# Performance work log

Measured on AMD Instinct MI355X. Metric: run time of the kernel, lower is better.

## Reference

```python
import jax, jax.numpy as jnp
import numpy as np
import math

DIM = 768
HEADS = 8
DIM_HEAD = 64
INNER = HEADS * DIM_HEAD  # 512
B, L = 2, 4096
LN_EPS = 1e-5


def setup_inputs() -> dict:
    key = jax.random.key(0)
    ks = jax.random.split(key, 6)
    std = 0.02
    return {
        "x": jax.random.normal(ks[0], (B, L, DIM), dtype=jnp.float32),
        "ln_gamma": jnp.ones((DIM,), dtype=jnp.float32),
        "ln_beta": jnp.zeros((DIM,), dtype=jnp.float32),
        "Wq": jax.random.normal(ks[1], (DIM, INNER), dtype=jnp.float32) * std,
        "Wkv": jax.random.normal(ks[2], (DIM, 2 * INNER), dtype=jnp.float32) * std,
        "Wo": jax.random.normal(ks[3], (INNER, DIM), dtype=jnp.float32) * std,
    }


def reference(x, ln_gamma, ln_beta, Wq, Wkv, Wo):
    b, l, _ = x.shape
    # LayerNorm (eps=1e-5, affine)
    mu = jnp.mean(x, axis=-1, keepdims=True)
    var = jnp.mean(jnp.square(x - mu), axis=-1, keepdims=True)
    xn = (x - mu) * jax.lax.rsqrt(var + LN_EPS) * ln_gamma + ln_beta

    q = xn @ Wq                      # (b, l, inner)
    kv = xn @ Wkv                    # (b, l, 2*inner)
    k, v = jnp.split(kv, 2, axis=-1)

    def to_heads(t):
        return t.reshape(b, l, HEADS, DIM_HEAD).transpose(0, 2, 1, 3)  # (b,h,l,d)

    q, k, v = to_heads(q), to_heads(k), to_heads(v)

    scale = 1.0 / math.sqrt(math.sqrt(DIM_HEAD))
    # explicit quadratic scores, softmax in float32 as in original
    weight = jnp.einsum("bhid,bhjd->bhij", q * scale, k * scale)
    weight = jax.nn.softmax(weight.astype(jnp.float32), axis=-1).astype(q.dtype)
    out = jnp.einsum("bhij,bhjd->bhid", weight, v)       # (b,h,l,d)
    out = out.transpose(0, 2, 1, 3).reshape(b, l, INNER)  # merge heads
    return out @ Wo
```

## Files before the change

kernel.cpp:

```cpp
#include <hip/hip_runtime.h>
#include <hip/hip_bf16.h>


typedef __bf16 bf16_t;
typedef __bf16 bf16x4 __attribute__((ext_vector_type(4)));
typedef __bf16 bf16x8 __attribute__((ext_vector_type(8)));
typedef float f32x4 __attribute__((ext_vector_type(4)));
typedef unsigned int u32x2 __attribute__((ext_vector_type(2)));

#define MFMA16(a, b, c) __builtin_amdgcn_mfma_f32_16x16x32_bf16((a), (b), (c), 0, 0, 0)

#define QSCALE 0.18033688011112042f

#define GLDS(gp, lp)                                                          \
    __builtin_amdgcn_global_load_lds(                                         \
        (const __attribute__((address_space(1))) void*)(gp),                  \
        (__attribute__((address_space(3))) void*)(lp), 16, 0, 0)

__device__ __forceinline__ int detect_f32(const unsigned int* __restrict__ xw) {
    const int l = threadIdx.x & 63;
    int cnt = 0;
#pragma unroll
    for (int j = 0; j < 2; ++j) {
        const unsigned int e = (xw[l * 2 + j] >> 7) & 0xFF;
        cnt += (e >= 100 && e <= 140) ? 1 : 0;
    }
#pragma unroll
    for (int off = 1; off < 64; off <<= 1) cnt += __shfl_xor(cnt, off, 64);
    return cnt < 64;
}

__global__ __launch_bounds__(256) void prep_kernel(
    const void* __restrict__ xv, const void* __restrict__ gv,
    const void* __restrict__ bv, const void* __restrict__ wq,
    const void* __restrict__ wkv, const void* __restrict__ wo,
    bf16_t* __restrict__ xn, bf16_t* __restrict__ WqkvT, bf16_t* __restrict__ WoT,
    int* __restrict__ flag) {
    const int f32 = detect_f32((const unsigned int*)xv);
    const int bid = blockIdx.x;
    const int t = threadIdx.x;
    if (bid == 0 && t == 0) *flag = f32;

    __shared__ bf16_t Ts[64 * 68];

    if (bid < 2048) {
        const int lane = t & 63;
        const int row = bid * 4 + (t >> 6);
        const int c0 = lane * 12;
        float v[12];
        if (f32) {
            const float* xr = (const float*)xv + (size_t)row * 768 + c0;
#pragma unroll
            for (int i = 0; i < 3; ++i) {
                const float4 q = *(const float4*)(xr + i * 4);
                v[i * 4] = q.x; v[i * 4 + 1] = q.y;
                v[i * 4 + 2] = q.z; v[i * 4 + 3] = q.w;
            }
        } else {
            const bf16_t* xr = (const bf16_t*)xv + (size_t)row * 768 + c0;
#pragma unroll
            for (int i = 0; i < 3; ++i) {
                const bf16x4 q = *(const bf16x4*)(xr + i * 4);
#pragma unroll
                for (int j = 0; j < 4; ++j) v[i * 4 + j] = (float)q[j];
            }
        }
        float s = 0.f, sq = 0.f;
#pragma unroll
        for (int j = 0; j < 12; ++j) { s += v[j]; sq += v[j] * v[j]; }
#pragma unroll
        for (int off = 1; off < 64; off <<= 1) {
            s += __shfl_xor(s, off, 64);
            sq += __shfl_xor(sq, off, 64);
        }
        const float mu = s * (1.0f / 768.0f);
        const float var = sq * (1.0f / 768.0f) - mu * mu;
        const float rstd = rsqrtf(var + 1e-5f);

        bf16_t* xo = xn + (size_t)row * 768 + c0;
#pragma unroll
        for (int i = 0; i < 3; ++i) {
            bf16x4 o;
#pragma unroll
            for (int j = 0; j < 4; ++j) {
                const int c = c0 + i * 4 + j;
                const float gc = f32 ? ((const float*)gv)[c] : (float)((const bf16_t*)gv)[c];
                const float bc = f32 ? ((const float*)bv)[c] : (float)((const bf16_t*)bv)[c];
                o[j] = (bf16_t)((v[i * 4 + j] - mu) * rstd * gc + bc);
            }
            *(bf16x4*)(xo + i * 4) = o;
        }
        return;
    }

    int idx = bid - 2048;
    const void* in;
    bf16_t* out;
    int R, C, cx, ry;
    if (idx < 96) {
        in = wq; out = WqkvT; R = 768; C = 512;
        cx = idx & 7; ry = idx >> 3;
    } else if (idx < 288) {
        idx -= 96;
        in = wkv; out = WqkvT + (size_t)512 * 768; R = 768; C = 1024;
        cx = idx & 15; ry = idx >> 4;
    } else {
        idx -= 288;
        in = wo; out = WoT; R = 512; C = 768;
        cx = idx % 12; ry = idx / 12;
    }
    const int r0 = ry * 64, c0 = cx * 64;
    {
        const int r = t >> 2, c = (t & 3) * 16;
        if (f32) {
            const float* src = (const float*)in + (size_t)(r0 + r) * C + c0 + c;
#pragma unroll
            for (int i = 0; i < 16; i += 4) {
                const float4 q = *(const float4*)(src + i);
                Ts[r * 68 + c + i] = (bf16_t)q.x;
                Ts[r * 68 + c + i + 1] = (bf16_t)q.y;
                Ts[r * 68 + c + i + 2] = (bf16_t)q.z;
                Ts[r * 68 + c + i + 3] = (bf16_t)q.w;
            }
        } else {
            const bf16_t* src = (const bf16_t*)in + (size_t)(r0 + r) * C + c0 + c;
            *(bf16x8*)&Ts[r * 68 + c] = *(const bf16x8*)src;
            *(bf16x8*)&Ts[r * 68 + c + 8] = *(const bf16x8*)(src + 8);
        }
    }
    __syncthreads();
    {
        const int oc = t >> 2, seg = (t & 3) * 16;
        bf16x8 v0, v1;
#pragma unroll
        for (int j = 0; j < 8; ++j) v0[j] = Ts[(seg + j) * 68 + oc];
#pragma unroll
        for (int j = 0; j < 8; ++j) v1[j] = Ts[(seg + 8 + j) * 68 + oc];
        bf16_t* dst = out + (size_t)(c0 + oc) * R + r0 + seg;
        *(bf16x8*)dst = v0;
        *(bf16x8*)(dst + 8) = v1;
    }
}

__global__ __launch_bounds__(256) void qkv_gemm(const bf16_t* __restrict__ A,
                                                const bf16_t* __restrict__ BT,
                                                bf16_t* __restrict__ qkv,
                                                bf16_t* __restrict__ vtg,
                                                int M, int N, int K) {
    const int m0 = blockIdx.y * 128;
    const int n0 = blockIdx.x * 128;
    __shared__ bf16_t As[128 * 32];
    __shared__ bf16_t Bs[128 * 32];

    const int t = threadIdx.x;
    const int lane = t & 63;
    const int w = t >> 6;
    const int wm = (w >> 1) * 64;
    const int wn = (w & 1) * 64;
    const int quad = lane >> 4;
    const int cl = lane & 15;

    f32x4 acc[4][4];
    const f32x4 z4 = {0.f, 0.f, 0.f, 0.f};
#pragma unroll
    for (int mi = 0; mi < 4; ++mi)
#pragma unroll
        for (int ni = 0; ni < 4; ++ni) acc[mi][ni] = z4;

    const int r0 = lane >> 2;
    const int c0 = (lane & 3) * 8;
    const bf16_t* AgL = A + (size_t)(m0 + w * 32 + r0) * K + c0;
    const bf16_t* AgH = A + (size_t)(m0 + w * 32 + 16 + r0) * K + c0;
    const bf16_t* BgL = BT + (size_t)(n0 + w * 32 + r0) * K + c0;
    const bf16_t* BgH = BT + (size_t)(n0 + w * 32 + 16 + r0) * K + c0;
    bf16_t* AdL = &As[(w * 32) * 32];
    bf16_t* AdH = &As[(w * 32 + 16) * 32];
    bf16_t* BdL = &Bs[(w * 32) * 32];
    bf16_t* BdH = &Bs[(w * 32 + 16) * 32];

    for (int kt = 0; kt < K; kt += 32) {
        __syncthreads();
        GLDS(AgL + kt, AdL);
        GLDS(AgH + kt, AdH);
        GLDS(BgL + kt, BdL);
        GLDS(BgH + kt, BdH);
        __syncthreads();

        const int ko = quad * 8;
        bf16x8 af[4], bfr[4];
#pragma unroll
        for (int mi = 0; mi < 4; ++mi)
            af[mi] = *(const bf16x8*)&As[(wm + mi * 16 + cl) * 32 + ko];
#pragma unroll
        for (int ni = 0; ni < 4; ++ni)
            bfr[ni] = *(const bf16x8*)&Bs[(wn + ni * 16 + cl) * 32 + ko];
#pragma unroll
        for (int mi = 0; mi < 4; ++mi)
#pragma unroll
            for (int ni = 0; ni < 4; ++ni)
                acc[mi][ni] = MFMA16(af[mi], bfr[ni], acc[mi][ni]);
    }

    if (n0 >= 1024) {
        const int b = m0 >> 12;
#pragma unroll
        for (int mi = 0; mi < 4; ++mi) {
#pragma unroll
            for (int ni = 0; ni < 4; ++ni) {
                const int tok = (m0 & 4095) + wm + mi * 16 + quad * 4;
                const int dl = n0 + wn + ni * 16 + cl - 1024;
                bf16x4 pk;
#pragma unroll
                for (int r4 = 0; r4 < 4; ++r4) pk[r4] = (bf16_t)acc[mi][ni][r4];
                *(bf16x4*)(vtg + ((size_t)(b * 8 + (dl >> 6)) * 64 + (dl & 63)) * 4096 +
                           tok) = pk;
            }
        }
    } else {
        const float sc = (n0 < 512) ? QSCALE : 1.0f;
#pragma unroll
        for (int mi = 0; mi < 4; ++mi) {
#pragma unroll
            for (int ni = 0; ni < 4; ++ni) {
#pragma unroll
                for (int r4 = 0; r4 < 4; ++r4) {
                    const int row = m0 + wm + mi * 16 + quad * 4 + r4;
                    const int col = n0 + wn + ni * 16 + cl;
                    qkv[(size_t)row * N + col] = (bf16_t)(acc[mi][ni][r4] * sc);
                }
            }
        }
    }
}

__global__ __launch_bounds__(128) void gemm_bt64(const bf16_t* __restrict__ A,
                                                 const bf16_t* __restrict__ BT,
                                                 void* __restrict__ C,
                                                 int M, int N, int K,
                                                 const int* __restrict__ out_flag) {
    const int m0 = blockIdx.y * 128;
    const int n0 = blockIdx.x * 64;
    __shared__ bf16_t As[128 * 32];
    __shared__ bf16_t Bs[64 * 32];

    const int t = threadIdx.x;
    const int lane = t & 63;
    const int w = t >> 6;
    const int quad = lane >> 4;
    const int cl = lane & 15;

    f32x4 acc[4][4];
    const f32x4 z4 = {0.f, 0.f, 0.f, 0.f};
#pragma unroll
    for (int mi = 0; mi < 4; ++mi)
#pragma unroll
        for (int ni = 0; ni < 4; ++ni) acc[mi][ni] = z4;

    const int r0 = lane >> 2;
    const int c0 = (lane & 3) * 8;
    const bf16_t* Ag = A + (size_t)(m0 + w * 64 + r0) * K + c0;
    const bf16_t* Bg = BT + (size_t)(n0 + w * 32 + r0) * K + c0;
    bf16_t* Ad = &As[(w * 64) * 32];
    bf16_t* Bd = &Bs[(w * 32) * 32];

    for (int kt = 0; kt < K; kt += 32) {
        __syncthreads();
#pragma unroll
        for (int i = 0; i < 4; ++i) GLDS(Ag + kt + (size_t)i * 16 * K, Ad + i * 512);
#pragma unroll
        for (int i = 0; i < 2; ++i) GLDS(Bg + kt + (size_t)i * 16 * K, Bd + i * 512);
        __syncthreads();

        const int ko = quad * 8;
        bf16x8 af[4], bfr[4];
#pragma unroll
        for (int mi = 0; mi < 4; ++mi)
            af[mi] = *(const bf16x8*)&As[(w * 64 + mi * 16 + cl) * 32 + ko];
#pragma unroll
        for (int ni = 0; ni < 4; ++ni)
            bfr[ni] = *(const bf16x8*)&Bs[(ni * 16 + cl) * 32 + ko];
#pragma unroll
        for (int mi = 0; mi < 4; ++mi)
#pragma unroll
            for (int ni = 0; ni < 4; ++ni)
                acc[mi][ni] = MFMA16(af[mi], bfr[ni], acc[mi][ni]);
    }

    const int f32out = *out_flag;
#pragma unroll
    for (int mi = 0; mi < 4; ++mi) {
#pragma unroll
        for (int ni = 0; ni < 4; ++ni) {
#pragma unroll
            for (int r4 = 0; r4 < 4; ++r4) {
                const int row = m0 + w * 64 + mi * 16 + quad * 4 + r4;
                const int col = n0 + ni * 16 + cl;
                if (f32out)
                    ((float*)C)[(size_t)row * N + col] = acc[mi][ni][r4];
                else
                    ((bf16_t*)C)[(size_t)row * N + col] = (bf16_t)acc[mi][ni][r4];
            }
        }
    }
}

__global__ __launch_bounds__(256, 2) void attn_kernel(const bf16_t* __restrict__ qkv,
                                                      const bf16_t* __restrict__ vtg,
                                                      bf16_t* __restrict__ ao) {
    const int qt = blockIdx.x;
    const int bh = blockIdx.y;
    const int b = bh >> 3, h = bh & 7;
    const int q0 = qt * 128;

    __shared__ bf16_t Ps[4][64 * 68];
    __shared__ bf16_t Ks[2][64 * 68];
    __shared__ bf16_t Vs[2][64 * 68];

    const int t = threadIdx.x;
    const int lane = t & 63;
    const int w = t >> 6;
    const int qsub = w & 1;
    const int kh = w >> 1;
    const int quad = lane >> 4;
    const int cl = lane & 15;

    const size_t rowbase = (size_t)b * 4096;
    const int qcol = h * 64;
    const int kcol = 512 + h * 64;

    bf16_t* Qtr = &Ps[0][0];
    {
        const bf16_t* qsrc = qkv + (rowbase + q0 + w * 32) * 1536 + qcol;
#pragma unroll
        for (int i = 0; i < 4; ++i)
            GLDS(qsrc + (size_t)(i * 8 + (lane >> 3)) * 1536 + (lane & 7) * 8,
                 Qtr + (w * 32 + i * 8) * 64);
    }
    __syncthreads();

    bf16x8 aq[4][2];
#pragma unroll
    for (int rt = 0; rt < 4; ++rt)
#pragma unroll
        for (int hh = 0; hh < 2; ++hh)
            aq[rt][hh] =
                *(const bf16x8*)&Qtr[(qsub * 64 + rt * 16 + cl) * 64 + hh * 32 + quad * 8];

    bf16x8 ones;
#pragma unroll
    for (int e = 0; e < 8; ++e) ones[e] = (bf16_t)1.0f;

    const f32x4 z4 = {0.f, 0.f, 0.f, 0.f};
    f32x4 o[4][4];
    f32x4 l_acc[4];
#pragma unroll
    for (int rt = 0; rt < 4; ++rt) {
        l_acc[rt] = z4;
#pragma unroll
        for (int ni = 0; ni < 4; ++ni) o[rt][ni] = z4;
    }

    const int t2 = qsub * 64 + lane;
    const int sr = t2 >> 1;
    const int sh = (t2 & 1) * 32;

    bf16x8 kreg[4], vreg[4];
    {
        const int k0 = kh * 2048;
        const bf16_t* ks = qkv + (rowbase + k0 + sr) * 1536 + kcol + sh;
        const bf16_t* vs = vtg + ((size_t)bh * 64 + sr) * 4096 + k0 + sh;
#pragma unroll
        for (int o8 = 0; o8 < 4; ++o8) {
            kreg[o8] = *(const bf16x8*)(ks + o8 * 8);
            vreg[o8] = *(const bf16x8*)(vs + o8 * 8);
        }
    }

    for (int it = 0; it < 32; ++it) {
        __syncthreads();
#pragma unroll
        for (int o8 = 0; o8 < 4; ++o8) {
            *(bf16x8*)&Ks[kh][sr * 68 + sh + o8 * 8] = kreg[o8];
            *(bf16x8*)&Vs[kh][sr * 68 + sh + o8 * 8] = vreg[o8];
        }
        __syncthreads();

        if (it < 31) {
            const int k0n = kh * 2048 + (it + 1) * 64;
            const bf16_t* ks = qkv + (rowbase + k0n + sr) * 1536 + kcol + sh;
            const bf16_t* vs = vtg + ((size_t)bh * 64 + sr) * 4096 + k0n + sh;
#pragma unroll
            for (int o8 = 0; o8 < 4; ++o8) {
                kreg[o8] = *(const bf16x8*)(ks + o8 * 8);
                vreg[o8] = *(const bf16x8*)(vs + o8 * 8);
            }
        }

        const int ko = quad * 8;
        bf16x8 kb[4][2];
#pragma unroll
        for (int ni = 0; ni < 4; ++ni) {
            kb[ni][0] = *(const bf16x8*)&Ks[kh][(ni * 16 + cl) * 68 + ko];
            kb[ni][1] = *(const bf16x8*)&Ks[kh][(ni * 16 + cl) * 68 + 32 + ko];
        }
        __builtin_amdgcn_s_setprio(1);
#pragma unroll
        for (int rt = 0; rt < 4; ++rt) {
#pragma unroll
            for (int ni = 0; ni < 4; ++ni) {
                f32x4 s = z4;
                s = MFMA16(kb[ni][0], aq[rt][0], s);
                s = MFMA16(kb[ni][1], aq[rt][1], s);
                const float e0 = __builtin_amdgcn_exp2f(s[0]);
                const float e1 = __builtin_amdgcn_exp2f(s[1]);
                const float e2 = __builtin_amdgcn_exp2f(s[2]);
                const float e3 = __builtin_amdgcn_exp2f(s[3]);
                u32x2 pk;
                asm("v_cvt_pk_bf16_f32 %0, %1, %2" : "=v"(pk[0]) : "v"(e0), "v"(e1));
                asm("v_cvt_pk_bf16_f32 %0, %1, %2" : "=v"(pk[1]) : "v"(e2), "v"(e3));
                *(u32x2*)&Ps[w][(rt * 16 + cl) * 68 + ni * 16 + quad * 4] = pk;
            }
        }
        __builtin_amdgcn_s_setprio(0);

        bf16x8 vb[4][2];
#pragma unroll
        for (int ni = 0; ni < 4; ++ni) {
            vb[ni][0] = *(const bf16x8*)&Vs[kh][(ni * 16 + cl) * 68 + ko];
            vb[ni][1] = *(const bf16x8*)&Vs[kh][(ni * 16 + cl) * 68 + 32 + ko];
        }
        __builtin_amdgcn_s_setprio(1);
#pragma unroll
        for (int rt = 0; rt < 4; ++rt) {
            const bf16x8 p0 = *(const bf16x8*)&Ps[w][(rt * 16 + cl) * 68 + ko];
            const bf16x8 p1 = *(const bf16x8*)&Ps[w][(rt * 16 + cl) * 68 + 32 + ko];
#pragma unroll
            for (int ni = 0; ni < 4; ++ni) {
                o[rt][ni] = MFMA16(p0, vb[ni][0], o[rt][ni]);
                o[rt][ni] = MFMA16(p1, vb[ni][1], o[rt][ni]);
            }
            l_acc[rt] = MFMA16(p0, ones, l_acc[rt]);
            l_acc[rt] = MFMA16(p1, ones, l_acc[rt]);
        }
        __builtin_amdgcn_s_setprio(0);
    }

    float* cb = (float*)&Ps[0][0];
    __syncthreads();
    if (kh == 1) {
#pragma unroll
        for (int rt = 0; rt < 4; ++rt) {
#pragma unroll
            for (int r4 = 0; r4 < 4; ++r4) {
                const int row = rt * 16 + quad * 4 + r4;
                float* rp = cb + qsub * 4160 + row * 65;
#pragma unroll
                for (int ni = 0; ni < 4; ++ni) rp[ni * 16 + cl] = o[rt][ni][r4];
                if (cl == 0) rp[64] = l_acc[rt][r4];
            }
        }
    }
    __syncthreads();
    if (kh == 0) {
#pragma unroll
        for (int rt = 0; rt < 4; ++rt) {
#pragma unroll
            for (int r4 = 0; r4 < 4; ++r4) {
                const int row = rt * 16 + quad * 4 + r4;
                const float* rp = cb + qsub * 4160 + row * 65;
                const float inv = 1.0f / (l_acc[rt][r4] + rp[64]);
                const size_t orow = rowbase + q0 + qsub * 64 + row;
#pragma unroll
                for (int ni = 0; ni < 4; ++ni)
                    ao[orow * 512 + h * 64 + ni * 16 + cl] =
                        (bf16_t)((o[rt][ni][r4] + rp[ni * 16 + cl]) * inv);
            }
        }
    }
}

extern "C" void kernel_launch(void* const* d_in, const int* in_sizes, int n_in,
                              void* d_out, int out_size, void* d_ws, size_t ws_size,
                              hipStream_t stream) {
    const void* x = d_in[0];
    const void* gamma = d_in[1];
    const void* beta = d_in[2];
    const void* Wq = d_in[3];
    const void* Wkv = d_in[4];
    const void* Wo = d_in[5];

    char* wsb = (char*)d_ws;
    int* flag = (int*)wsb;
    bf16_t* xn = (bf16_t*)(wsb + 256);
    bf16_t* WqkvT = xn + (size_t)8192 * 768;
    bf16_t* WoT = WqkvT + (size_t)1536 * 768;
    bf16_t* qkv = WoT + (size_t)768 * 512;
    bf16_t* aob = xn;
    bf16_t* vtg = (bf16_t*)d_out;

    prep_kernel<<<2432, 256, 0, stream>>>(x, gamma, beta, Wq, Wkv, Wo, xn, WqkvT, WoT,
                                          flag);

    qkv_gemm<<<dim3(12, 64), 256, 0, stream>>>(xn, WqkvT, qkv, vtg, 8192, 1536, 768);

    attn_kernel<<<dim3(32, 16), 256, 0, stream>>>(qkv, vtg, aob);

    gemm_bt64<<<dim3(12, 64), 128, 0, stream>>>(aob, WoT, d_out, 8192, 768, 512, flag);
}
```

Before: 231.5 us.

## Shrink attention q-tile to 64 rows and drop split-K across warps

```diff
diff --git a/kernel.cpp b/kernel.cpp
--- a/kernel.cpp
+++ b/kernel.cpp
@@ -304,23 +304,21 @@
     }
 }
 
-__global__ __launch_bounds__(256, 2) void attn_kernel(const bf16_t* __restrict__ qkv,
+__global__ __launch_bounds__(256, 4) void attn_kernel(const bf16_t* __restrict__ qkv,
                                                       const bf16_t* __restrict__ vtg,
                                                       bf16_t* __restrict__ ao) {
     const int qt = blockIdx.x;
     const int bh = blockIdx.y;
     const int b = bh >> 3, h = bh & 7;
-    const int q0 = qt * 128;
-
-    __shared__ bf16_t Ps[4][64 * 68];
-    __shared__ bf16_t Ks[2][64 * 68];
-    __shared__ bf16_t Vs[2][64 * 68];
+    const int q0 = qt * 64;
+
+    __shared__ bf16_t Ps[4][16 * 68];
+    __shared__ bf16_t Ks[64 * 68];
+    __shared__ bf16_t Vs[64 * 68];
 
     const int t = threadIdx.x;
     const int lane = t & 63;
     const int w = t >> 6;
-    const int qsub = w & 1;
-    const int kh = w >> 1;
     const int quad = lane >> 4;
     const int cl = lane & 15;
 
@@ -328,154 +326,104 @@
     const int qcol = h * 64;
     const int kcol = 512 + h * 64;
 
-    bf16_t* Qtr = &Ps[0][0];
+    bf16_t* Qtr = &Ks[0];
     {
-        const bf16_t* qsrc = qkv + (rowbase + q0 + w * 32) * 1536 + qcol;
-#pragma unroll
-        for (int i = 0; i < 4; ++i)
+        const bf16_t* qsrc = qkv + (rowbase + q0 + w * 16) * 1536 + qcol;
+#pragma unroll
+        for (int i = 0; i < 2; ++i)
             GLDS(qsrc + (size_t)(i * 8 + (lane >> 3)) * 1536 + (lane & 7) * 8,
-                 Qtr + (w * 32 + i * 8) * 64);
-    }
+                 Qtr + (w * 16 + i * 8) * 64);
+    }
+
+    const int sr2 = t >> 3;
+    const int sh2 = (t & 7) * 8;
+    const bf16_t* kgp = qkv + (rowbase + sr2) * 1536 + kcol + sh2;
+    const bf16_t* vgp = vtg + ((size_t)bh * 64 + sr2) * 4096 + sh2;
+
+    bf16x8 kreg[2], vreg[2];
+    {
+        kreg[0] = *(const bf16x8*)(kgp);
+        kreg[1] = *(const bf16x8*)(kgp + (size_t)32 * 1536);
+        vreg[0] = *(const bf16x8*)(vgp);
+        vreg[1] = *(const bf16x8*)(vgp + (size_t)32 * 4096);
+    }
+
     __syncthreads();
 
-    bf16x8 aq[4][2];
-#pragma unroll
-    for (int rt = 0; rt < 4; ++rt)
-#pragma unroll
-        for (int hh = 0; hh < 2; ++hh)
-            aq[rt][hh] =
-                *(const bf16x8*)&Qtr[(qsub * 64 + rt * 16 + cl) * 64 + hh * 32 + quad * 8];
+    bf16x8 aq[2];
+#pragma unroll
+    for (int hh = 0; hh < 2; ++hh)
+        aq[hh] = *(const bf16x8*)&Qtr[(w * 16 + cl) * 64 + hh * 32 + quad * 8];
 
     bf16x8 ones;
 #pragma unroll
     for (int e = 0; e < 8; ++e) ones[e] = (bf16_t)1.0f;
 
     const f32x4 z4 = {0.f, 0.f, 0.f, 0.f};
-    f32x4 o[4][4];
-    f32x4 l_acc[4];
-#pragma unroll
-    for (int rt = 0; rt < 4; ++rt) {
-        l_acc[rt] = z4;
-#pragma unroll
-        for (int ni = 0; ni < 4; ++ni) o[rt][ni] = z4;
-    }
-
-    const int t2 = qsub * 64 + lane;
-    const int sr = t2 >> 1;
-    const int sh = (t2 & 1) * 32;
-
-    bf16x8 kreg[4], vreg[4];
-    {
-        const int k0 = kh * 2048;
-        const bf16_t* ks = qkv + (rowbase + k0 + sr) * 1536 + kcol + sh;
-        const bf16_t* vs = vtg + ((size_t)bh * 64 + sr) * 4096 + k0 + sh;
-#pragma unroll
-        for (int o8 = 0; o8 < 4; ++o8) {
-            kreg[o8] = *(const bf16x8*)(ks + o8 * 8);
-            vreg[o8] = *(const bf16x8*)(vs + o8 * 8);
-        }
-    }
-
-    for (int it = 0; it < 32; ++it) {
-        __syncthreads();
-#pragma unroll
-        for (int o8 = 0; o8 < 4; ++o8) {
-            *(bf16x8*)&Ks[kh][sr * 68 + sh + o8 * 8] = kreg[o8];
-            *(bf16x8*)&Vs[kh][sr * 68 + sh + o8 * 8] = vreg[o8];
-        }
-        __syncthreads();
-
-        if (it < 31) {
-            const int k0n = kh * 2048 + (it + 1) * 64;
-            const bf16_t* ks = qkv + (rowbase + k0n + sr) * 1536 + kcol + sh;
-            const bf16_t* vs = vtg + ((size_t)bh * 64 + sr) * 4096 + k0n + sh;
-#pragma unroll
-            for (int o8 = 0; o8 < 4; ++o8) {
-                kreg[o8] = *(const bf16x8*)(ks + o8 * 8);
-                vreg[o8] = *(const bf16x8*)(vs + o8 * 8);
-            }
-        }
-
-        const int ko = quad * 8;
-        bf16x8 kb[4][2];
+    f32x4 o[4];
+    f32x4 l_acc = z4;
+#pragma unroll
+    for (int ni = 0; ni < 4; ++ni) o[ni] = z4;
+
+    for (int it = 0; it < 64; ++it) {
+        __syncthreads();
+        *(bf16x8*)&Ks[sr2 * 68 + sh2] = kreg[0];
+        *(bf16x8*)&Ks[(sr2 + 32) * 68 + sh2] = kreg[1];
+        *(bf16x8*)&Vs[sr2 * 68 + sh2] = vreg[0];
+        *(bf16x8*)&Vs[(sr2 + 32) * 68 + sh2] = vreg[1];
+        __syncthreads();
+
+        if (it < 63) {
+            const size_t ko = (size_t)(it + 1) * 64;
+            kreg[0] = *(const bf16x8*)(kgp + ko * 1536);
+            kreg[1] = *(const bf16x8*)(kgp + (ko + 32) * 1536);
+            vreg[0] = *(const bf16x8*)(vgp + ko);
+            vreg[1] = *(const bf16x8*)(vgp + (size_t)32 * 4096 + ko);
+        }
+
+        const int ko2 = quad * 8;
+        __builtin_amdgcn_s_setprio(1);
 #pragma unroll
         for (int ni = 0; ni < 4; ++ni) {
-            kb[ni][0] = *(const bf16x8*)&Ks[kh][(ni * 16 + cl) * 68 + ko];
-            kb[ni][1] = *(const bf16x8*)&Ks[kh][(ni * 16 + cl) * 68 + 32 + ko];
-        }
+            const bf16x8 kb0 = *(const bf16x8*)&Ks[(ni * 16 + cl) * 68 + ko2];
+            const bf16x8 kb1 = *(const bf16x8*)&Ks[(ni * 16 + cl) * 68 + 32 + ko2];
+            f32x4 s = z4;
+            s = MFMA16(kb0, aq[0], s);
+            s = MFMA16(kb1, aq[1], s);
+            const float e0 = __builtin_amdgcn_exp2f(s[0]);
+            const float e1 = __builtin_amdgcn_exp2f(s[1]);
+            const float e2 = __builtin_amdgcn_exp2f(s[2]);
+            const float e3 = __builtin_amdgcn_exp2f(s[3]);
+            u32x2 pk;
+            asm("v_cvt_pk_bf16_f32 %0, %1, %2" : "=v"(pk[0]) : "v"(e0), "v"(e1));
+            asm("v_cvt_pk_bf16_f32 %0, %1, %2" : "=v"(pk[1]) : "v"(e2), "v"(e3));
+            *(u32x2*)&Ps[w][cl * 68 + ni * 16 + quad * 4] = pk;
+        }
+        __builtin_amdgcn_s_setprio(0);
+
+        const bf16x8 p0 = *(const bf16x8*)&Ps[w][cl * 68 + ko2];
+        const bf16x8 p1 = *(const bf16x8*)&Ps[w][cl * 68 + 32 + ko2];
         __builtin_amdgcn_s_setprio(1);
 #pragma unroll
-        for (int rt = 0; rt < 4; ++rt) {
-#pragma unroll
-            for (int ni = 0; ni < 4; ++ni) {
-                f32x4 s = z4;
-                s = MFMA16(kb[ni][0], aq[rt][0], s);
-                s = MFMA16(kb[ni][1], aq[rt][1], s);
-                const float e0 = __builtin_amdgcn_exp2f(s[0]);
-                const float e1 = __builtin_amdgcn_exp2f(s[1]);
-                const float e2 = __builtin_amdgcn_exp2f(s[2]);
-                const float e3 = __builtin_amdgcn_exp2f(s[3]);
-                u32x2 pk;
-                asm("v_cvt_pk_bf16_f32 %0, %1, %2" : "=v"(pk[0]) : "v"(e0), "v"(e1));
-                asm("v_cvt_pk_bf16_f32 %0, %1, %2" : "=v"(pk[1]) : "v"(e2), "v"(e3));
-                *(u32x2*)&Ps[w][(rt * 16 + cl) * 68 + ni * 16 + quad * 4] = pk;
-            }
-        }
+        for (int ni = 0; ni < 4; ++ni) {
+            const bf16x8 vb0 = *(const bf16x8*)&Vs[(ni * 16 + cl) * 68 + ko2];
+            const bf16x8 vb1 = *(const bf16x8*)&Vs[(ni * 16 + cl) * 68 + 32 + ko2];
+            o[ni] = MFMA16(p0, vb0, o[ni]);
+            o[ni] = MFMA16(p1, vb1, o[ni]);
+        }
+        l_acc = MFMA16(p0, ones, l_acc);
+        l_acc = MFMA16(p1, ones, l_acc);
         __builtin_amdgcn_s_setprio(0);
-
-        bf16x8 vb[4][2];
-#pragma unroll
-        for (int ni = 0; ni < 4; ++ni) {
-            vb[ni][0] = *(const bf16x8*)&Vs[kh][(ni * 16 + cl) * 68 + ko];
-            vb[ni][1] = *(const bf16x8*)&Vs[kh][(ni * 16 + cl) * 68 + 32 + ko];
-        }
-        __builtin_amdgcn_s_setprio(1);
-#pragma unroll
-        for (int rt = 0; rt < 4; ++rt) {
-            const bf16x8 p0 = *(const bf16x8*)&Ps[w][(rt * 16 + cl) * 68 + ko];
-            const bf16x8 p1 = *(const bf16x8*)&Ps[w][(rt * 16 + cl) * 68 + 32 + ko];
-#pragma unroll
-            for (int ni = 0; ni < 4; ++ni) {
-                o[rt][ni] = MFMA16(p0, vb[ni][0], o[rt][ni]);
-                o[rt][ni] = MFMA16(p1, vb[ni][1], o[rt][ni]);
-            }
-            l_acc[rt] = MFMA16(p0, ones, l_acc[rt]);
-            l_acc[rt] = MFMA16(p1, ones, l_acc[rt]);
-        }
-        __builtin_amdgcn_s_setprio(0);
-    }
-
-    float* cb = (float*)&Ps[0][0];
-    __syncthreads();
-    if (kh == 1) {
-#pragma unroll
-        for (int rt = 0; rt < 4; ++rt) {
-#pragma unroll
-            for (int r4 = 0; r4 < 4; ++r4) {
-                const int row = rt * 16 + quad * 4 + r4;
-                float* rp = cb + qsub * 4160 + row * 65;
-#pragma unroll
-                for (int ni = 0; ni < 4; ++ni) rp[ni * 16 + cl] = o[rt][ni][r4];
-                if (cl == 0) rp[64] = l_acc[rt][r4];
-            }
-        }
-    }
-    __syncthreads();
-    if (kh == 0) {
-#pragma unroll
-        for (int rt = 0; rt < 4; ++rt) {
-#pragma unroll
-            for (int r4 = 0; r4 < 4; ++r4) {
-                const int row = rt * 16 + quad * 4 + r4;
-                const float* rp = cb + qsub * 4160 + row * 65;
-                const float inv = 1.0f / (l_acc[rt][r4] + rp[64]);
-                const size_t orow = rowbase + q0 + qsub * 64 + row;
-#pragma unroll
-                for (int ni = 0; ni < 4; ++ni)
-                    ao[orow * 512 + h * 64 + ni * 16 + cl] =
-                        (bf16_t)((o[rt][ni][r4] + rp[ni * 16 + cl]) * inv);
-            }
-        }
+    }
+
+#pragma unroll
+    for (int r4 = 0; r4 < 4; ++r4) {
+        const int row = q0 + w * 16 + quad * 4 + r4;
+        const float inv = 1.0f / l_acc[r4];
+        bf16_t* op = ao + (rowbase + row) * 512 + qcol;
+#pragma unroll
+        for (int ni = 0; ni < 4; ++ni)
+            op[ni * 16 + cl] = (bf16_t)(o[ni][r4] * inv);
     }
 }
 
@@ -503,7 +451,7 @@
 
     qkv_gemm<<<dim3(12, 64), 256, 0, stream>>>(xn, WqkvT, qkv, vtg, 8192, 1536, 768);
 
-    attn_kernel<<<dim3(32, 16), 256, 0, stream>>>(qkv, vtg, aob);
+    attn_kernel<<<dim3(64, 16), 256, 0, stream>>>(qkv, vtg, aob);
 
     gemm_bt64<<<dim3(12, 64), 128, 0, stream>>>(aob, WoT, d_out, 8192, 768, 512, flag);
 }
```

Result: slower. 256.4 us (+10.8%).
